# Kernel optimization log

Measured on AMD Instinct MI355X. Metric: run time of the kernel, lower is better.

Reference implementation:

```python
import jax, jax.numpy as jnp
import numpy as np

B, S, D, H, E, TOPK = 4, 2048, 1024, 2048, 8, 2


def setup_inputs() -> dict:
    key = jax.random.key(0)
    ks = jax.random.split(key, 5)
    scale_d = 1.0 / np.sqrt(D)
    scale_h = 1.0 / np.sqrt(H)
    return {
        "hidden_states": jax.random.normal(ks[0], (B, S, D), dtype=jnp.float32),
        "router_w": jax.random.normal(ks[1], (E, D), dtype=jnp.float32) * scale_d,  # logits = x @ router_w.T
        "w_gate": jax.random.normal(ks[2], (E, H, D), dtype=jnp.float32) * scale_d,
        "w_up": jax.random.normal(ks[3], (E, H, D), dtype=jnp.float32) * scale_d,
        "w_down": jax.random.normal(ks[4], (E, D, H), dtype=jnp.float32) * scale_h,
    }


def reference(hidden_states, router_w, w_gate, w_up, w_down):
    b, s, d = hidden_states.shape
    x = hidden_states.reshape(-1, d)                      # [T, D]
    T = x.shape[0]

    router_logits = x @ router_w.T                        # [T, E]
    router_probs = jax.nn.softmax(router_logits.astype(jnp.float32), axis=-1)
    topk_w, topk_idx = jax.lax.top_k(router_probs, TOPK)  # [T, K]
    topk_w = topk_w / jnp.sum(topk_w, axis=-1, keepdims=True)

    # combine[t, e] = renormalized routing weight of token t for expert e (0 if not selected)
    combine = jnp.zeros((T, E), dtype=topk_w.dtype)
    combine = combine.at[jnp.arange(T)[:, None], topk_idx].add(topk_w)

    # Dense all-expert SwiGLU (correctness baseline; combine zeros out unselected experts)
    g = jnp.einsum('td,ehd->teh', x, w_gate)              # [T, E, H]
    u = jnp.einsum('td,ehd->teh', x, w_up)                # [T, E, H]
    h = jax.nn.silu(g) * u                                # [T, E, H]
    y = jnp.einsum('teh,edh->ted', h, w_down)             # [T, E, D]
    out = jnp.einsum('te,ted->td', combine.astype(y.dtype), y)
    return out.reshape(b, s, d)
```

## Files before the change

### kernel.cpp

```cpp
#include <hip/hip_runtime.h>
#include <hip/hip_bf16.h>
#include <stdint.h>

#define T_TOK 8192
#define D_DIM 1024
#define H_DIM 2048
#define E_NUM 8
#define KSEL  2
#define NROWS (T_TOK*KSEL)

#define BM 128
#define BN 128
#define BK 64

typedef __bf16 bf16_t;
typedef bf16_t bf16x8 __attribute__((ext_vector_type(8)));
typedef float  f32x4  __attribute__((ext_vector_type(4)));

__device__ __forceinline__ ushort f2bf(float f) {
    uint32_t u = __builtin_bit_cast(uint32_t, f);
    uint32_t r = (u + 0x7FFFu + ((u >> 16) & 1u)) >> 16;
    return (ushort)r;
}

__device__ __forceinline__ void gload16(const ushort* g, ushort* l) {
    __builtin_amdgcn_global_load_lds(
        (const __attribute__((address_space(1))) void*)g,
        (__attribute__((address_space(3))) void*)l, 16, 0, 0);
}

__global__ __launch_bounds__(256) void convert_kernel(const float* __restrict__ src,
                                                      ushort* __restrict__ dst, int n4) {
    int i = blockIdx.x * 256 + threadIdx.x;
    int stride = gridDim.x * 256;
    for (; i < n4; i += stride) {
        float4 v = *(const float4*)(src + (size_t)i * 4);
        ushort4 o;
        o.x = f2bf(v.x); o.y = f2bf(v.y); o.z = f2bf(v.z); o.w = f2bf(v.w);
        *(ushort4*)(dst + (size_t)i * 4) = o;
    }
}

__global__ __launch_bounds__(256) void router_kernel(const float* __restrict__ x,
                                                     const float* __restrict__ rw,
                                                     ushort* __restrict__ x16,
                                                     int* __restrict__ topk_idx,
                                                     float* __restrict__ topk_w,
                                                     int* __restrict__ cnt) {
    const int wid  = threadIdx.x >> 6;
    const int lane = threadIdx.x & 63;
    const int t = blockIdx.x * 4 + wid;
    const float* xr = x + (size_t)t * D_DIM;

    float acc[E_NUM];
#pragma unroll
    for (int e = 0; e < E_NUM; e++) acc[e] = 0.f;

#pragma unroll
    for (int i = 0; i < 4; i++) {
        int d0 = i * 256 + lane * 4;
        float4 xv = *(const float4*)(xr + d0);
        ushort4 o;
        o.x = f2bf(xv.x); o.y = f2bf(xv.y); o.z = f2bf(xv.z); o.w = f2bf(xv.w);
        *(ushort4*)(x16 + (size_t)t * D_DIM + d0) = o;
#pragma unroll
        for (int e = 0; e < E_NUM; e++) {
            float4 wv = *(const float4*)(rw + e * D_DIM + d0);
            acc[e] += xv.x * wv.x + xv.y * wv.y + xv.z * wv.z + xv.w * wv.w;
        }
    }
#pragma unroll
    for (int e = 0; e < E_NUM; e++) {
#pragma unroll
        for (int s = 32; s > 0; s >>= 1) acc[e] += __shfl_xor(acc[e], s);
    }
    int e1 = 0; float m1 = acc[0];
#pragma unroll
    for (int e = 1; e < E_NUM; e++) if (acc[e] > m1) { m1 = acc[e]; e1 = e; }
    int e2 = -1; float m2 = -INFINITY;
#pragma unroll
    for (int e = 0; e < E_NUM; e++) if (e != e1 && acc[e] > m2) { m2 = acc[e]; e2 = e; }
    float w1 = 1.f / (1.f + expf(m2 - m1));
    float w2 = 1.f - w1;
    if (lane == 0) {
        topk_idx[t * 2 + 0] = e1; topk_idx[t * 2 + 1] = e2;
        topk_w  [t * 2 + 0] = w1; topk_w  [t * 2 + 1] = w2;
        atomicAdd(cnt + e1, 1);
        atomicAdd(cnt + e2, 1);
    }
}

__global__ void prefix_kernel(const int* __restrict__ cnt, int* __restrict__ offs,
                              int* __restrict__ fill) {
    if (threadIdx.x == 0) {
        int s = 0;
        for (int e = 0; e < E_NUM; e++) { offs[e] = s; fill[e] = s; s += cnt[e]; }
        offs[E_NUM] = s;
    }
}

__global__ __launch_bounds__(256) void scatter_kernel(const int* __restrict__ topk_idx,
                                                      int* __restrict__ fill,
                                                      int* __restrict__ row_token,
                                                      int* __restrict__ rowmap) {
    int t = blockIdx.x * 256 + threadIdx.x;
#pragma unroll
    for (int k = 0; k < KSEL; k++) {
        int e = topk_idx[t * 2 + k];
        int pos = atomicAdd(fill + e, 1);
        row_token[pos] = t;
        rowmap[t * 2 + k] = pos;
    }
}

__global__ __launch_bounds__(512) void gateup_kernel(const ushort* __restrict__ x16,
                                                     const ushort* __restrict__ wg16,
                                                     const ushort* __restrict__ wu16,
                                                     const int* __restrict__ offs,
                                                     const int* __restrict__ row_token,
                                                     ushort* __restrict__ h16) {
    const int e = blockIdx.z;
    const int off_e = offs[e];
    const int n_e = offs[e + 1] - off_e;
    const int m0 = blockIdx.y * BM;
    if (m0 >= n_e) return;
    const int n0 = blockIdx.x * BN;

    __shared__ __align__(16) ushort sA[BM * BK];
    __shared__ __align__(16) ushort sBg[BN * BK];
    __shared__ __align__(16) ushort sBu[BN * BK];
    __shared__ int sTok[BM];

    const int tid = threadIdx.x;
    if (tid < BM) {
        int r = m0 + tid;
        sTok[tid] = row_token[off_e + (r < n_e ? r : n_e - 1)];
    }
    __syncthreads();

    const int wid = tid >> 6, lane = tid & 63;
    const int s0 = wid * 2, s1 = s0 + 1;
    const int lrow = lane >> 3;
    const int lcol = lane & 7;
    const int xc = ((lcol ^ lrow) * 8);
    const int rA0 = s0 * 8 + lrow, rA1 = s1 * 8 + lrow;

    const ushort* gA0 = x16 + (size_t)sTok[rA0] * D_DIM + xc;
    const ushort* gA1 = x16 + (size_t)sTok[rA1] * D_DIM + xc;
    const ushort* gG0 = wg16 + ((size_t)e * H_DIM + n0 + rA0) * D_DIM + xc;
    const ushort* gG1 = wg16 + ((size_t)e * H_DIM + n0 + rA1) * D_DIM + xc;
    const ushort* gU0 = wu16 + ((size_t)e * H_DIM + n0 + rA0) * D_DIM + xc;
    const ushort* gU1 = wu16 + ((size_t)e * H_DIM + n0 + rA1) * D_DIM + xc;
    ushort* lA0 = sA  + s0 * 512; ushort* lA1 = sA  + s1 * 512;
    ushort* lG0 = sBg + s0 * 512; ushort* lG1 = sBg + s1 * 512;
    ushort* lU0 = sBu + s0 * 512; ushort* lU1 = sBu + s1 * 512;

    const int wr = wid >> 2, wc = wid & 3;
    const int fr = lane & 15, fq = lane >> 4;

    f32x4 accg[4][2], accu[4][2];
    f32x4 z4 = {0.f, 0.f, 0.f, 0.f};
#pragma unroll
    for (int m = 0; m < 4; m++)
#pragma unroll
        for (int n = 0; n < 2; n++) { accg[m][n] = z4; accu[m][n] = z4; }

    const int NKT = D_DIM / BK;
    for (int kt = 0; kt < NKT; ++kt) {
        gload16(gA0, lA0); gload16(gA1, lA1);
        gload16(gG0, lG0); gload16(gG1, lG1);
        gload16(gU0, lU0); gload16(gU1, lU1);
        gA0 += BK; gA1 += BK; gG0 += BK; gG1 += BK; gU0 += BK; gU1 += BK;
        __syncthreads();
#pragma unroll
        for (int ks = 0; ks < 2; ++ks) {
            bf16x8 af[4], bg[2], bu[2];
#pragma unroll
            for (int m = 0; m < 4; m++) {
                int r = wr * 64 + m * 16 + fr;
                af[m] = *(const bf16x8*)&sA[r * BK + (((ks * 4 + fq) ^ (r & 7)) * 8)];
            }
#pragma unroll
            for (int n = 0; n < 2; n++) {
                int c = wc * 32 + n * 16 + fr;
                int sl = ((ks * 4 + fq) ^ (c & 7)) * 8;
                bg[n] = *(const bf16x8*)&sBg[c * BK + sl];
                bu[n] = *(const bf16x8*)&sBu[c * BK + sl];
            }
#pragma unroll
            for (int m = 0; m < 4; m++)
#pragma unroll
                for (int n = 0; n < 2; n++) {
                    accg[m][n] = __builtin_amdgcn_mfma_f32_16x16x32_bf16(af[m], bg[n], accg[m][n], 0, 0, 0);
                    accu[m][n] = __builtin_amdgcn_mfma_f32_16x16x32_bf16(af[m], bu[n], accu[m][n], 0, 0, 0);
                }
        }
        __syncthreads();
    }

#pragma unroll
    for (int m = 0; m < 4; m++)
#pragma unroll
        for (int n = 0; n < 2; n++) {
            int col = n0 + wc * 32 + n * 16 + fr;
#pragma unroll
            for (int v = 0; v < 4; v++) {
                int grow = m0 + wr * 64 + m * 16 + fq * 4 + v;
                if (grow < n_e) {
                    float g = accg[m][n][v], u = accu[m][n][v];
                    float h = g / (1.f + expf(-g)) * u;
                    h16[(size_t)(off_e + grow) * H_DIM + col] = f2bf(h);
                }
            }
        }
}

__global__ __launch_bounds__(512) void down_kernel(const ushort* __restrict__ h16,
                                                   const ushort* __restrict__ wd16,
                                                   const int* __restrict__ offs,
                                                   float* __restrict__ y) {
    const int e = blockIdx.z;
    const int off_e = offs[e];
    const int n_e = offs[e + 1] - off_e;
    const int m0 = blockIdx.y * BM;
    if (m0 >= n_e) return;
    const int n0 = blockIdx.x * BN;

    __shared__ __align__(16) ushort sA[BM * BK];
    __shared__ __align__(16) ushort sB[BN * BK];

    const int tid = threadIdx.x;
    const int wid = tid >> 6, lane = tid & 63;
    const int s0 = wid * 2, s1 = s0 + 1;
    const int lrow = lane >> 3;
    const int lcol = lane & 7;
    const int xc = ((lcol ^ lrow) * 8);
    int ar0 = m0 + s0 * 8 + lrow; if (ar0 >= n_e) ar0 = n_e - 1;
    int ar1 = m0 + s1 * 8 + lrow; if (ar1 >= n_e) ar1 = n_e - 1;

    const ushort* gA0 = h16 + (size_t)(off_e + ar0) * H_DIM + xc;
    const ushort* gA1 = h16 + (size_t)(off_e + ar1) * H_DIM + xc;
    const ushort* gB0 = wd16 + ((size_t)e * D_DIM + n0 + s0 * 8 + lrow) * H_DIM + xc;
    const ushort* gB1 = wd16 + ((size_t)e * D_DIM + n0 + s1 * 8 + lrow) * H_DIM + xc;
    ushort* lA0 = sA + s0 * 512; ushort* lA1 = sA + s1 * 512;
    ushort* lB0 = sB + s0 * 512; ushort* lB1 = sB + s1 * 512;

    const int wr = wid >> 2, wc = wid & 3;
    const int fr = lane & 15, fq = lane >> 4;

    f32x4 acc[4][2];
    f32x4 z4 = {0.f, 0.f, 0.f, 0.f};
#pragma unroll
    for (int m = 0; m < 4; m++)
#pragma unroll
        for (int n = 0; n < 2; n++) acc[m][n] = z4;

    const int NKT = H_DIM / BK;
    for (int kt = 0; kt < NKT; ++kt) {
        gload16(gA0, lA0); gload16(gA1, lA1);
        gload16(gB0, lB0); gload16(gB1, lB1);
        gA0 += BK; gA1 += BK; gB0 += BK; gB1 += BK;
        __syncthreads();
#pragma unroll
        for (int ks = 0; ks < 2; ++ks) {
            bf16x8 af[4], bf[2];
#pragma unroll
            for (int m = 0; m < 4; m++) {
                int r = wr * 64 + m * 16 + fr;
                af[m] = *(const bf16x8*)&sA[r * BK + (((ks * 4 + fq) ^ (r & 7)) * 8)];
            }
#pragma unroll
            for (int n = 0; n < 2; n++) {
                int c = wc * 32 + n * 16 + fr;
                bf[n] = *(const bf16x8*)&sB[c * BK + (((ks * 4 + fq) ^ (c & 7)) * 8)];
            }
#pragma unroll
            for (int m = 0; m < 4; m++)
#pragma unroll
                for (int n = 0; n < 2; n++)
                    acc[m][n] = __builtin_amdgcn_mfma_f32_16x16x32_bf16(af[m], bf[n], acc[m][n], 0, 0, 0);
        }
        __syncthreads();
    }

#pragma unroll
    for (int m = 0; m < 4; m++)
#pragma unroll
        for (int n = 0; n < 2; n++) {
            int col = n0 + wc * 32 + n * 16 + fr;
#pragma unroll
            for (int v = 0; v < 4; v++) {
                int grow = m0 + wr * 64 + m * 16 + fq * 4 + v;
                if (grow < n_e)
                    y[(size_t)(off_e + grow) * D_DIM + col] = acc[m][n][v];
            }
        }
}

__global__ __launch_bounds__(256) void combine_kernel(const float* __restrict__ y,
                                                      const int* __restrict__ rowmap,
                                                      const float* __restrict__ topk_w,
                                                      float* __restrict__ out) {
    const int t = blockIdx.x;
    const int d = threadIdx.x * 4;
    const int r0 = rowmap[t * 2], r1 = rowmap[t * 2 + 1];
    const float w0 = topk_w[t * 2], w1 = topk_w[t * 2 + 1];
    float4 a = *(const float4*)(y + (size_t)r0 * D_DIM + d);
    float4 b = *(const float4*)(y + (size_t)r1 * D_DIM + d);
    float4 o;
    o.x = w0 * a.x + w1 * b.x;
    o.y = w0 * a.y + w1 * b.y;
    o.z = w0 * a.z + w1 * b.z;
    o.w = w0 * a.w + w1 * b.w;
    *(float4*)(out + (size_t)t * D_DIM + d) = o;
}

extern "C" void kernel_launch(void* const* d_in, const int* in_sizes, int n_in,
                              void* d_out, int out_size, void* d_ws, size_t ws_size,
                              hipStream_t stream) {
    const float* x  = (const float*)d_in[0];
    const float* rw = (const float*)d_in[1];
    const float* wg = (const float*)d_in[2];
    const float* wu = (const float*)d_in[3];
    const float* wd = (const float*)d_in[4];
    float* out = (float*)d_out;

    char* p = (char*)d_ws;
    size_t off = 0;
    auto alloc = [&](size_t b) { size_t c = off; off = (off + b + 255) & ~(size_t)255; return c; };
    size_t ctrl_o = alloc(256);
    size_t tki_o  = alloc((size_t)T_TOK * KSEL * 4);
    size_t tkw_o  = alloc((size_t)T_TOK * KSEL * 4);
    size_t rtok_o = alloc((size_t)NROWS * 4);
    size_t rmap_o = alloc((size_t)NROWS * 4);
    size_t x16_o  = alloc((size_t)T_TOK * D_DIM * 2);
    size_t wg16_o = alloc((size_t)E_NUM * H_DIM * D_DIM * 2);
    size_t wu16_o = alloc((size_t)E_NUM * H_DIM * D_DIM * 2);
    size_t wd16_o = alloc((size_t)E_NUM * D_DIM * H_DIM * 2);
    size_t h16_o  = alloc((size_t)NROWS * H_DIM * 2);
    if (off > ws_size) return;

    int*    cnt       = (int*)(p + ctrl_o);
    int*    offs      = (int*)(p + ctrl_o + 64);
    int*    fill      = (int*)(p + ctrl_o + 128);
    int*    topk_idx  = (int*)(p + tki_o);
    float*  topk_w    = (float*)(p + tkw_o);
    int*    row_token = (int*)(p + rtok_o);
    int*    rowmap    = (int*)(p + rmap_o);
    ushort* x16  = (ushort*)(p + x16_o);
    ushort* wg16 = (ushort*)(p + wg16_o);
    ushort* wu16 = (ushort*)(p + wu16_o);
    ushort* wd16 = (ushort*)(p + wd16_o);
    ushort* h16  = (ushort*)(p + h16_o);
    float*  y    = (float*)(p + wg16_o);

    hipMemsetAsync(p + ctrl_o, 0, 256, stream);

    const int n4w = (E_NUM * H_DIM * D_DIM) / 4;
    convert_kernel<<<1024, 256, 0, stream>>>(wg, wg16, n4w);
    convert_kernel<<<1024, 256, 0, stream>>>(wu, wu16, n4w);
    convert_kernel<<<1024, 256, 0, stream>>>(wd, wd16, n4w);

    router_kernel<<<T_TOK / 4, 256, 0, stream>>>(x, rw, x16, topk_idx, topk_w, cnt);
    prefix_kernel<<<1, 64, 0, stream>>>(cnt, offs, fill);
    scatter_kernel<<<T_TOK / 256, 256, 0, stream>>>(topk_idx, fill, row_token, rowmap);

    gateup_kernel<<<dim3(H_DIM / BN, T_TOK / BM, E_NUM), 512, 0, stream>>>(
        x16, wg16, wu16, offs, row_token, h16);
    down_kernel<<<dim3(D_DIM / BN, T_TOK / BM, E_NUM), 512, 0, stream>>>(
        h16, wd16, offs, y);
    combine_kernel<<<T_TOK, 256, 0, stream>>>(y, rowmap, topk_w, out);
}
```

Before: 863.0 us.

## Double-buffer LDS tiles in gate/up and down GEMMs with MFMA priority boost

Both grouped GEMM kernels now keep two LDS buffers per operand. The global-to-LDS loads for the next K tile are issued before the MFMAs on the current tile, instead of load-then-sync every iteration. This is meant to hide global load latency behind matrix math and removes one barrier per iteration. MFMA blocks are also wrapped in s_setprio to favour the compute waves. In exchange, LDS per block doubles (about 96KB for gate/up), which can reduce how many blocks fit on each CU.

```diff
diff --git a/kernel.cpp b/kernel.cpp
--- a/kernel.cpp
+++ b/kernel.cpp
@@ -12,6 +12,7 @@
 #define BM 128
 #define BN 128
 #define BK 64
+#define TILE_ELTS (BM*BK)
 
 typedef __bf16 bf16_t;
 typedef bf16_t bf16x8 __attribute__((ext_vector_type(8)));
@@ -126,9 +127,9 @@
     if (m0 >= n_e) return;
     const int n0 = blockIdx.x * BN;
 
-    __shared__ __align__(16) ushort sA[BM * BK];
-    __shared__ __align__(16) ushort sBg[BN * BK];
-    __shared__ __align__(16) ushort sBu[BN * BK];
+    __shared__ __align__(16) ushort sA [2 * TILE_ELTS];
+    __shared__ __align__(16) ushort sBg[2 * TILE_ELTS];
+    __shared__ __align__(16) ushort sBu[2 * TILE_ELTS];
     __shared__ int sTok[BM];
 
     const int tid = threadIdx.x;
@@ -151,9 +152,7 @@
     const ushort* gG1 = wg16 + ((size_t)e * H_DIM + n0 + rA1) * D_DIM + xc;
     const ushort* gU0 = wu16 + ((size_t)e * H_DIM + n0 + rA0) * D_DIM + xc;
     const ushort* gU1 = wu16 + ((size_t)e * H_DIM + n0 + rA1) * D_DIM + xc;
-    ushort* lA0 = sA  + s0 * 512; ushort* lA1 = sA  + s1 * 512;
-    ushort* lG0 = sBg + s0 * 512; ushort* lG1 = sBg + s1 * 512;
-    ushort* lU0 = sBu + s0 * 512; ushort* lU1 = sBu + s1 * 512;
+    const int o0 = s0 * 512, o1 = s1 * 512;
 
     const int wr = wid >> 2, wc = wid & 3;
     const int fr = lane & 15, fq = lane >> 4;
@@ -165,28 +164,41 @@
 #pragma unroll
         for (int n = 0; n < 2; n++) { accg[m][n] = z4; accu[m][n] = z4; }
 
+    gload16(gA0, sA  + o0); gload16(gA1, sA  + o1);
+    gload16(gG0, sBg + o0); gload16(gG1, sBg + o1);
+    gload16(gU0, sBu + o0); gload16(gU1, sBu + o1);
+    gA0 += BK; gA1 += BK; gG0 += BK; gG1 += BK; gU0 += BK; gU1 += BK;
+    __syncthreads();
+
     const int NKT = D_DIM / BK;
     for (int kt = 0; kt < NKT; ++kt) {
-        gload16(gA0, lA0); gload16(gA1, lA1);
-        gload16(gG0, lG0); gload16(gG1, lG1);
-        gload16(gU0, lU0); gload16(gU1, lU1);
-        gA0 += BK; gA1 += BK; gG0 += BK; gG1 += BK; gU0 += BK; gU1 += BK;
-        __syncthreads();
+        const int cur = (kt & 1) * TILE_ELTS;
+        const int nxt = TILE_ELTS - cur;
+        if (kt + 1 < NKT) {
+            gload16(gA0, sA  + nxt + o0); gload16(gA1, sA  + nxt + o1);
+            gload16(gG0, sBg + nxt + o0); gload16(gG1, sBg + nxt + o1);
+            gload16(gU0, sBu + nxt + o0); gload16(gU1, sBu + nxt + o1);
+            gA0 += BK; gA1 += BK; gG0 += BK; gG1 += BK; gU0 += BK; gU1 += BK;
+        }
+        const ushort* cA  = sA  + cur;
+        const ushort* cBg = sBg + cur;
+        const ushort* cBu = sBu + cur;
 #pragma unroll
         for (int ks = 0; ks < 2; ++ks) {
             bf16x8 af[4], bg[2], bu[2];
 #pragma unroll
             for (int m = 0; m < 4; m++) {
                 int r = wr * 64 + m * 16 + fr;
-                af[m] = *(const bf16x8*)&sA[r * BK + (((ks * 4 + fq) ^ (r & 7)) * 8)];
+                af[m] = *(const bf16x8*)&cA[r * BK + (((ks * 4 + fq) ^ (r & 7)) * 8)];
             }
 #pragma unroll
             for (int n = 0; n < 2; n++) {
                 int c = wc * 32 + n * 16 + fr;
                 int sl = ((ks * 4 + fq) ^ (c & 7)) * 8;
-                bg[n] = *(const bf16x8*)&sBg[c * BK + sl];
-                bu[n] = *(const bf16x8*)&sBu[c * BK + sl];
-            }
+                bg[n] = *(const bf16x8*)&cBg[c * BK + sl];
+                bu[n] = *(const bf16x8*)&cBu[c * BK + sl];
+            }
+            __builtin_amdgcn_s_setprio(1);
 #pragma unroll
             for (int m = 0; m < 4; m++)
 #pragma unroll
@@ -194,6 +206,7 @@
                     accg[m][n] = __builtin_amdgcn_mfma_f32_16x16x32_bf16(af[m], bg[n], accg[m][n], 0, 0, 0);
                     accu[m][n] = __builtin_amdgcn_mfma_f32_16x16x32_bf16(af[m], bu[n], accu[m][n], 0, 0, 0);
                 }
+            __builtin_amdgcn_s_setprio(0);
         }
         __syncthreads();
     }
@@ -226,8 +239,8 @@
     if (m0 >= n_e) return;
     const int n0 = blockIdx.x * BN;
 
-    __shared__ __align__(16) ushort sA[BM * BK];
-    __shared__ __align__(16) ushort sB[BN * BK];
+    __shared__ __align__(16) ushort sA[2 * TILE_ELTS];
+    __shared__ __align__(16) ushort sB[2 * TILE_ELTS];
 
     const int tid = threadIdx.x;
     const int wid = tid >> 6, lane = tid & 63;
@@ -242,8 +255,7 @@
     const ushort* gA1 = h16 + (size_t)(off_e + ar1) * H_DIM + xc;
     const ushort* gB0 = wd16 + ((size_t)e * D_DIM + n0 + s0 * 8 + lrow) * H_DIM + xc;
     const ushort* gB1 = wd16 + ((size_t)e * D_DIM + n0 + s1 * 8 + lrow) * H_DIM + xc;
-    ushort* lA0 = sA + s0 * 512; ushort* lA1 = sA + s1 * 512;
-    ushort* lB0 = sB + s0 * 512; ushort* lB1 = sB + s1 * 512;
+    const int o0 = s0 * 512, o1 = s1 * 512;
 
     const int wr = wid >> 2, wc = wid & 3;
     const int fr = lane & 15, fq = lane >> 4;
@@ -255,30 +267,42 @@
 #pragma unroll
         for (int n = 0; n < 2; n++) acc[m][n] = z4;
 
+    gload16(gA0, sA + o0); gload16(gA1, sA + o1);
+    gload16(gB0, sB + o0); gload16(gB1, sB + o1);
+    gA0 += BK; gA1 += BK; gB0 += BK; gB1 += BK;
+    __syncthreads();
+
     const int NKT = H_DIM / BK;
     for (int kt = 0; kt < NKT; ++kt) {
-        gload16(gA0, lA0); gload16(gA1, lA1);
-        gload16(gB0, lB0); gload16(gB1, lB1);
-        gA0 += BK; gA1 += BK; gB0 += BK; gB1 += BK;
-        __syncthreads();
+        const int cur = (kt & 1) * TILE_ELTS;
+        const int nxt = TILE_ELTS - cur;
+        if (kt + 1 < NKT) {
+            gload16(gA0, sA + nxt + o0); gload16(gA1, sA + nxt + o1);
+            gload16(gB0, sB + nxt + o0); gload16(gB1, sB + nxt + o1);
+            gA0 += BK; gA1 += BK; gB0 += BK; gB1 += BK;
+        }
+        const ushort* cA = sA + cur;
+        const ushort* cB = sB + cur;
 #pragma unroll
         for (int ks = 0; ks < 2; ++ks) {
             bf16x8 af[4], bf[2];
 #pragma unroll
             for (int m = 0; m < 4; m++) {
                 int r = wr * 64 + m * 16 + fr;
-                af[m] = *(const bf16x8*)&sA[r * BK + (((ks * 4 + fq) ^ (r & 7)) * 8)];
+                af[m] = *(const bf16x8*)&cA[r * BK + (((ks * 4 + fq) ^ (r & 7)) * 8)];
             }
 #pragma unroll
             for (int n = 0; n < 2; n++) {
                 int c = wc * 32 + n * 16 + fr;
-                bf[n] = *(const bf16x8*)&sB[c * BK + (((ks * 4 + fq) ^ (c & 7)) * 8)];
-            }
+                bf[n] = *(const bf16x8*)&cB[c * BK + (((ks * 4 + fq) ^ (c & 7)) * 8)];
+            }
+            __builtin_amdgcn_s_setprio(1);
 #pragma unroll
             for (int m = 0; m < 4; m++)
 #pragma unroll
                 for (int n = 0; n < 2; n++)
                     acc[m][n] = __builtin_amdgcn_mfma_f32_16x16x32_bf16(af[m], bf[n], acc[m][n], 0, 0, 0);
+            __builtin_amdgcn_s_setprio(0);
         }
         __syncthreads();
     }
```

Measured after the change: 868.9 us. No clear change (+0.7%).
